# Kernel optimization log

Measured on AMD Instinct MI355X. Metric: run time of the kernel, lower is better.

Reference implementation:

```python
import jax, jax.numpy as jnp
import numpy as np

IN_FEATURES = 256
OUT_FEATURES = 128
ALPHA = 0.2  # LeakyReLU negative slope
NEG_INF = -9e15
N_NODES = 8192


def _xavier_uniform(key, shape, gain):
    fan_in, fan_out = shape[0], shape[1]
    limit = gain * np.sqrt(6.0 / (fan_in + fan_out))
    return jax.random.uniform(key, shape, jnp.float32, -limit, limit)


def setup_inputs() -> dict:
    key = jax.random.key(0)
    k_h, k_adj, k_W, k_a = jax.random.split(key, 4)
    h = jax.random.normal(k_h, (N_NODES, IN_FEATURES), dtype=jnp.float32)
    adj = jax.random.randint(k_adj, (N_NODES, N_NODES), 0, 2, dtype=jnp.int32)
    W = _xavier_uniform(k_W, (IN_FEATURES, OUT_FEATURES), gain=1.414)
    a = _xavier_uniform(k_a, (2 * OUT_FEATURES, 1), gain=1.414)
    return {"h": h, "adj": adj, "W": W, "a": a}


def reference(h, adj, W, a):
    # Wh: (N, F_out)
    Wh = h @ W
    # Decompose a = [a1; a2]; e_ij = leakyrelu(Wh_i . a1 + Wh_j . a2)
    # == the original concat([Wh_i, Wh_j]) @ a, without the O(N^2*2F) tensor.
    a1 = a[:OUT_FEATURES, 0]  # (F_out,)
    a2 = a[OUT_FEATURES:, 0]  # (F_out,)
    src = Wh @ a1  # (N,)
    dst = Wh @ a2  # (N,)
    e = jax.nn.leaky_relu(src[:, None] + dst[None, :], negative_slope=ALPHA)  # (N, N)
    attention = jnp.where(adj > 0, e, NEG_INF)
    attention = jax.nn.softmax(attention, axis=1)
    # dropout p=0.0 (eval) -> identity
    h_prime = attention @ Wh  # (N, F_out)
    return jax.nn.elu(h_prime)  # concat=True
```

## Files before the change

### kernel.cpp

```cpp
#include <hip/hip_runtime.h>

#define N_NODES 8192
#define IN_F    256
#define OUT_F   128
#define ALPHA_S 0.2f

typedef __attribute__((ext_vector_type(8))) short  short8;
typedef __attribute__((ext_vector_type(4))) short  short4v;
typedef __attribute__((ext_vector_type(4))) float  floatx4;
typedef __attribute__((ext_vector_type(4))) int    intx4;
typedef __attribute__((ext_vector_type(4))) float  fx4;

static __device__ __forceinline__ short f2bf(float f) {
    union { float f; unsigned int i; } u; u.f = f;
    unsigned int r = u.i + 0x7FFFu + ((u.i >> 16) & 1u);
    return (short)(r >> 16);
}

__global__ __launch_bounds__(512) void k_wh(
    const float* __restrict__ h,
    const float* __restrict__ W,
    const float* __restrict__ a,
    short* __restrict__ WhT,
    float* __restrict__ src,
    float* __restrict__ dst)
{
    __shared__ short Wt[OUT_F][IN_F + 8];
    __shared__ short htile[32][IN_F + 8];
    __shared__ float q1s[IN_F], q2s[IN_F];
    __shared__ short wh_t[OUT_F][40];

    const int t      = threadIdx.x;
    const int lane   = t & 63;
    const int wave   = t >> 6;
    const int r_base = blockIdx.x * 32;

#pragma unroll
    for (int rep = 0; rep < 4; ++rep) {
        const int idx = rep * 8192 + t * 16;
        const int k   = idx >> 7;
        const int f   = idx & 127;
        fx4 w0 = *(const fx4*)(W + idx);
        fx4 w1 = *(const fx4*)(W + idx + 4);
        fx4 w2 = *(const fx4*)(W + idx + 8);
        fx4 w3 = *(const fx4*)(W + idx + 12);
        fx4 a10 = *(const fx4*)(a + f);
        fx4 a11 = *(const fx4*)(a + f + 4);
        fx4 a12 = *(const fx4*)(a + f + 8);
        fx4 a13 = *(const fx4*)(a + f + 12);
        fx4 a20 = *(const fx4*)(a + OUT_F + f);
        fx4 a21 = *(const fx4*)(a + OUT_F + f + 4);
        fx4 a22 = *(const fx4*)(a + OUT_F + f + 8);
        fx4 a23 = *(const fx4*)(a + OUT_F + f + 12);
        float p1 = 0.f, p2 = 0.f;
#pragma unroll
        for (int e = 0; e < 4; ++e) {
            p1 = fmaf(w0[e], a10[e], p1); p2 = fmaf(w0[e], a20[e], p2);
            p1 = fmaf(w1[e], a11[e], p1); p2 = fmaf(w1[e], a21[e], p2);
            p1 = fmaf(w2[e], a12[e], p1); p2 = fmaf(w2[e], a22[e], p2);
            p1 = fmaf(w3[e], a13[e], p1); p2 = fmaf(w3[e], a23[e], p2);
        }
#pragma unroll
        for (int e = 0; e < 4; ++e) {
            Wt[f + e][k]      = f2bf(w0[e]);
            Wt[f + 4 + e][k]  = f2bf(w1[e]);
            Wt[f + 8 + e][k]  = f2bf(w2[e]);
            Wt[f + 12 + e][k] = f2bf(w3[e]);
        }
#pragma unroll
        for (int m = 1; m < 8; m <<= 1) {
            p1 += __shfl_xor(p1, m, 64);
            p2 += __shfl_xor(p2, m, 64);
        }
        if ((t & 7) == 0) { q1s[k] = p1; q2s[k] = p2; }
    }

    const int r0   = t >> 4;
    const int fgrp = t & 15;
    const int k0   = fgrp * 16;
    fx4 h0, h1, h2, h3;
    {
        const float* hp = h + (size_t)(r_base + r0) * IN_F + k0;
        h0 = *(const fx4*)hp; h1 = *(const fx4*)(hp + 4);
        h2 = *(const fx4*)(hp + 8); h3 = *(const fx4*)(hp + 12);
        short8 b0, b1;
#pragma unroll
        for (int e = 0; e < 4; ++e) {
            b0[e]     = f2bf(h0[e]); b0[4 + e] = f2bf(h1[e]);
            b1[e]     = f2bf(h2[e]); b1[4 + e] = f2bf(h3[e]);
        }
        *(short8*)&htile[r0][k0]     = b0;
        *(short8*)&htile[r0][k0 + 8] = b1;
    }
    __syncthreads();

    {
        float sp = 0.f, dp = 0.f;
#pragma unroll
        for (int e = 0; e < 4; ++e) {
            sp = fmaf(h0[e], q1s[k0 + e], sp);      dp = fmaf(h0[e], q2s[k0 + e], dp);
            sp = fmaf(h1[e], q1s[k0 + 4 + e], sp);  dp = fmaf(h1[e], q2s[k0 + 4 + e], dp);
            sp = fmaf(h2[e], q1s[k0 + 8 + e], sp);  dp = fmaf(h2[e], q2s[k0 + 8 + e], dp);
            sp = fmaf(h3[e], q1s[k0 + 12 + e], sp); dp = fmaf(h3[e], q2s[k0 + 12 + e], dp);
        }
#pragma unroll
        for (int m = 1; m < 16; m <<= 1) {
            sp += __shfl_xor(sp, m, 64);
            dp += __shfl_xor(dp, m, 64);
        }
        if (fgrp == 0) { src[r_base + r0] = sp; dst[r_base + r0] = dp; }
    }

    const int ln15 = lane & 15;
    const int q    = lane >> 4;
    const int f0   = wave * 16;
    floatx4 c0 = {0.f, 0.f, 0.f, 0.f};
    floatx4 c1 = {0.f, 0.f, 0.f, 0.f};
#pragma unroll
    for (int s = 0; s < 8; ++s) {
        short8 bf  = *(const short8*)&Wt[f0 + ln15][s * 32 + q * 8];
        short8 a0f = *(const short8*)&htile[ln15][s * 32 + q * 8];
        short8 a1f = *(const short8*)&htile[16 + ln15][s * 32 + q * 8];
        c0 = __builtin_amdgcn_mfma_f32_16x16x32_bf16(a0f, bf, c0, 0, 0, 0);
        c1 = __builtin_amdgcn_mfma_f32_16x16x32_bf16(a1f, bf, c1, 0, 0, 0);
    }
    {
        short4v p0, p1;
#pragma unroll
        for (int r = 0; r < 4; ++r) { p0[r] = f2bf(c0[r]); p1[r] = f2bf(c1[r]); }
        *(short4v*)&wh_t[f0 + ln15][q * 4]      = p0;
        *(short4v*)&wh_t[f0 + ln15][16 + q * 4] = p1;
    }
    __syncthreads();
    {
        const int f    = t >> 2;
        const int half = t & 3;
        *(short8*)(WhT + (size_t)f * N_NODES + r_base + half * 8) =
            *(const short8*)&wh_t[f][half * 8];
    }
}

#define BM 32
#define BK 128
#define WPAD (BK + 8)
#define NIT (N_NODES / BK)

__global__ __launch_bounds__(1024, 4) void k_attn(
    const int*   __restrict__ adj,
    const short* __restrict__ WhT,
    const float* __restrict__ src,
    const float* __restrict__ dstv,
    float* __restrict__ out)
{
    __shared__ short wbuf[2][BM * WPAD];
    __shared__ float denom_s[BM];

    const int t    = threadIdx.x;
    const int lane = t & 63;
    const int wave = t >> 6;
    const int r0   = blockIdx.x * BM;

    const int sm  = t >> 5;
    const int sk0 = (t & 31) * 4;
    const float srow = src[r0 + sm];
    const int*   abase = adj  + (size_t)(r0 + sm) * N_NODES + sk0;
    const float* dbase = dstv + sk0;

    const int ln15 = lane & 15;
    const int q    = lane >> 4;
    const int rg   = wave >> 3;
    const int f0   = (wave & 7) * 16;
    const short* bbase = WhT + (size_t)(f0 + ln15) * N_NODES + q * 8;

    floatx4 acc = {0.f, 0.f, 0.f, 0.f};
    floatx4 dac = {0.f, 0.f, 0.f, 0.f};
    short8 ones;
#pragma unroll
    for (int j = 0; j < 8; ++j) ones[j] = (short)0x3F80;

    intx4 m0 = *(const intx4*)abase;
    fx4   d0 = *(const fx4*)dbase;

    for (int it = 0; it < NIT; ++it) {
        const int p = it & 1;
        short4v wv;
#pragma unroll
        for (int e = 0; e < 4; ++e) {
            float x = srow + d0[e];
            float l = fmaxf(x, ALPHA_S * x);
            wv[e] = (m0[e] > 0) ? f2bf(__expf(l)) : (short)0;
        }
        *(short4v*)&wbuf[p][sm * WPAD + sk0] = wv;
        if (it + 1 < NIT) {
            const int o = (it + 1) * BK;
            m0 = *(const intx4*)(abase + o);
            d0 = *(const fx4*)(dbase + o);
        }
        __syncthreads();
        const short* ab = &wbuf[p][(rg * 16 + ln15) * WPAD + q * 8];
        const short* bb = bbase + it * BK;
#pragma unroll
        for (int ks = 0; ks < 4; ++ks) {
            short8 afr = *(const short8*)(ab + ks * 32);
            short8 bfr = *(const short8*)(bb + ks * 32);
            acc = __builtin_amdgcn_mfma_f32_16x16x32_bf16(afr, bfr, acc, 0, 0, 0);
            if ((wave & 7) == 0)
                dac = __builtin_amdgcn_mfma_f32_16x16x32_bf16(afr, ones, dac, 0, 0, 0);
        }
    }

    if ((wave & 7) == 0 && ln15 == 0) {
#pragma unroll
        for (int r = 0; r < 4; ++r) denom_s[rg * 16 + q * 4 + r] = dac[r];
    }
    __syncthreads();

    float* op = out + (size_t)(r0 + rg * 16) * OUT_F + f0 + ln15;
#pragma unroll
    for (int r = 0; r < 4; ++r) {
        float dn = denom_s[rg * 16 + q * 4 + r];
        float v  = acc[r];
        v = (dn != 0.f) ? (v / dn) : 0.f;
        v = v > 0.f ? v : (__expf(v) - 1.f);
        op[(size_t)(q * 4 + r) * OUT_F] = v;
    }
}

extern "C" void kernel_launch(void* const* d_in, const int* in_sizes, int n_in,
                              void* d_out, int out_size, void* d_ws, size_t ws_size,
                              hipStream_t stream) {
    const float* h   = (const float*)d_in[0];
    const int*   adj = (const int*)d_in[1];
    const float* W   = (const float*)d_in[2];
    const float* a   = (const float*)d_in[3];
    float* out = (float*)d_out;

    char*  ws  = (char*)d_ws;
    short* WhT = (short*)ws;
    float* src = (float*)(ws + (2 << 20));
    float* dst = src + N_NODES;

    k_wh  <<<256,  512, 0, stream>>>(h, W, a, WhT, src, dst);
    k_attn<<<256, 1024, 0, stream>>>(adj, WhT, src, dst, out);
}
```

Baseline: 455.2 us.

## Retile attention kernel to 16-row blocks with 2-deep prefetch and scalar denominators

```diff
diff --git a/kernel.cpp b/kernel.cpp
--- a/kernel.cpp
+++ b/kernel.cpp
@@ -15,6 +15,11 @@
     union { float f; unsigned int i; } u; u.f = f;
     unsigned int r = u.i + 0x7FFFu + ((u.i >> 16) & 1u);
     return (short)(r >> 16);
+}
+static __device__ __forceinline__ float bf2f(short s) {
+    union { float f; unsigned int i; } u;
+    u.i = ((unsigned int)(unsigned short)s) << 16;
+    return u.f;
 }
 
 __global__ __launch_bounds__(512) void k_wh(
@@ -140,12 +145,12 @@
     }
 }
 
-#define BM 32
-#define BK 128
+#define BM 16
+#define BK 256
 #define WPAD (BK + 8)
 #define NIT (N_NODES / BK)
 
-__global__ __launch_bounds__(1024, 4) void k_attn(
+__global__ __launch_bounds__(512, 4) void k_attn(
     const int*   __restrict__ adj,
     const short* __restrict__ WhT,
     const float* __restrict__ src,
@@ -153,7 +158,7 @@
     float* __restrict__ out)
 {
     __shared__ short wbuf[2][BM * WPAD];
-    __shared__ float denom_s[BM];
+    __shared__ float denom_acc[BM];
 
     const int t    = threadIdx.x;
     const int lane = t & 63;
@@ -161,64 +166,83 @@
     const int r0   = blockIdx.x * BM;
 
     const int sm  = t >> 5;
-    const int sk0 = (t & 31) * 4;
+    const int sk0 = (t & 31) * 8;
     const float srow = src[r0 + sm];
     const int*   abase = adj  + (size_t)(r0 + sm) * N_NODES + sk0;
     const float* dbase = dstv + sk0;
 
     const int ln15 = lane & 15;
     const int q    = lane >> 4;
-    const int rg   = wave >> 3;
-    const int f0   = (wave & 7) * 16;
+    const int f0   = wave * 16;
     const short* bbase = WhT + (size_t)(f0 + ln15) * N_NODES + q * 8;
 
+    if ((t & 31) == 0) denom_acc[sm] = 0.f;
+
     floatx4 acc = {0.f, 0.f, 0.f, 0.f};
-    floatx4 dac = {0.f, 0.f, 0.f, 0.f};
-    short8 ones;
-#pragma unroll
-    for (int j = 0; j < 8; ++j) ones[j] = (short)0x3F80;
-
-    intx4 m0 = *(const intx4*)abase;
-    fx4   d0 = *(const fx4*)dbase;
-
-    for (int it = 0; it < NIT; ++it) {
-        const int p = it & 1;
-        short4v wv;
-#pragma unroll
-        for (int e = 0; e < 4; ++e) {
-            float x = srow + d0[e];
-            float l = fmaxf(x, ALPHA_S * x);
-            wv[e] = (m0[e] > 0) ? f2bf(__expf(l)) : (short)0;
-        }
-        *(short4v*)&wbuf[p][sm * WPAD + sk0] = wv;
-        if (it + 1 < NIT) {
-            const int o = (it + 1) * BK;
-            m0 = *(const intx4*)(abase + o);
-            d0 = *(const fx4*)(dbase + o);
-        }
-        __syncthreads();
-        const short* ab = &wbuf[p][(rg * 16 + ln15) * WPAD + q * 8];
-        const short* bb = bbase + it * BK;
-#pragma unroll
-        for (int ks = 0; ks < 4; ++ks) {
-            short8 afr = *(const short8*)(ab + ks * 32);
-            short8 bfr = *(const short8*)(bb + ks * 32);
-            acc = __builtin_amdgcn_mfma_f32_16x16x32_bf16(afr, bfr, acc, 0, 0, 0);
-            if ((wave & 7) == 0)
-                dac = __builtin_amdgcn_mfma_f32_16x16x32_bf16(afr, ones, dac, 0, 0, 0);
-        }
-    }
-
-    if ((wave & 7) == 0 && ln15 == 0) {
-#pragma unroll
-        for (int r = 0; r < 4; ++r) denom_s[rg * 16 + q * 4 + r] = dac[r];
-    }
+
+    intx4 mA0 = *(const intx4*)abase;
+    intx4 mA1 = *(const intx4*)(abase + 4);
+    fx4   dA0 = *(const fx4*)dbase;
+    fx4   dA1 = *(const fx4*)(dbase + 4);
+    intx4 mB0 = *(const intx4*)(abase + BK);
+    intx4 mB1 = *(const intx4*)(abase + BK + 4);
+    fx4   dB0 = *(const fx4*)(dbase + BK);
+    fx4   dB1 = *(const fx4*)(dbase + BK + 4);
+
+#define ATTN_STEP(IT, P, M0, M1, D0, D1)                                      \
+    {                                                                         \
+        short8 wv;                                                            \
+        float rsum = 0.f;                                                     \
+        _Pragma("unroll") for (int e = 0; e < 4; ++e) {                       \
+            float x = srow + D0[e];                                           \
+            float l = fmaxf(x, ALPHA_S * x);                                  \
+            short b = (M0[e] > 0) ? f2bf(__expf(l)) : (short)0;               \
+            wv[e] = b; rsum += bf2f(b);                                       \
+        }                                                                     \
+        _Pragma("unroll") for (int e = 0; e < 4; ++e) {                       \
+            float x = srow + D1[e];                                           \
+            float l = fmaxf(x, ALPHA_S * x);                                  \
+            short b = (M1[e] > 0) ? f2bf(__expf(l)) : (short)0;               \
+            wv[4 + e] = b; rsum += bf2f(b);                                   \
+        }                                                                     \
+        *(short8*)&wbuf[P][sm * WPAD + sk0] = wv;                             \
+        _Pragma("unroll") for (int m = 1; m < 32; m <<= 1)                    \
+            rsum += __shfl_xor(rsum, m, 64);                                  \
+        if ((t & 31) == 0) denom_acc[sm] += rsum;                             \
+        if ((IT) + 2 < NIT) {                                                 \
+            const int o = ((IT) + 2) * BK;                                    \
+            M0 = *(const intx4*)(abase + o);                                  \
+            M1 = *(const intx4*)(abase + o + 4);                              \
+            D0 = *(const fx4*)(dbase + o);                                    \
+            D1 = *(const fx4*)(dbase + o + 4);                                \
+        }                                                                     \
+        short8 bfr[8];                                                        \
+        const short* bb = bbase + (IT) * BK;                                  \
+        _Pragma("unroll") for (int ks = 0; ks < 8; ++ks)                      \
+            bfr[ks] = *(const short8*)(bb + ks * 32);                         \
+        asm volatile("s_waitcnt lgkmcnt(0)" ::: "memory");                    \
+        __builtin_amdgcn_s_barrier();                                         \
+        asm volatile("" ::: "memory");                                        \
+        const short* ab = &wbuf[P][ln15 * WPAD + q * 8];                      \
+        _Pragma("unroll") for (int ks = 0; ks < 8; ++ks) {                    \
+            short8 afr = *(const short8*)(ab + ks * 32);                      \
+            acc = __builtin_amdgcn_mfma_f32_16x16x32_bf16(afr, bfr[ks], acc,  \
+                                                          0, 0, 0);           \
+        }                                                                     \
+    }
+
+    for (int it = 0; it < NIT; it += 2) {
+        ATTN_STEP(it,     0, mA0, mA1, dA0, dA1)
+        ATTN_STEP(it + 1, 1, mB0, mB1, dB0, dB1)
+    }
+#undef ATTN_STEP
+
     __syncthreads();
 
-    float* op = out + (size_t)(r0 + rg * 16) * OUT_F + f0 + ln15;
+    float* op = out + (size_t)r0 * OUT_F + f0 + ln15;
 #pragma unroll
     for (int r = 0; r < 4; ++r) {
-        float dn = denom_s[rg * 16 + q * 4 + r];
+        float dn = denom_acc[q * 4 + r];
         float v  = acc[r];
         v = (dn != 0.f) ? (v / dn) : 0.f;
         v = v > 0.f ? v : (__expf(v) - 1.f);
@@ -240,6 +264,6 @@
     float* src = (float*)(ws + (2 << 20));
     float* dst = src + N_NODES;
 
-    k_wh  <<<256,  512, 0, stream>>>(h, W, a, WhT, src, dst);
-    k_attn<<<256, 1024, 0, stream>>>(adj, WhT, src, dst, out);
-}
+    k_wh  <<<256, 512, 0, stream>>>(h, W, a, WhT, src, dst);
+    k_attn<<<512, 512, 0, stream>>>(adj, WhT, src, dst, out);
+}
```

Result: faster. 426.3 us (-6.3%).
